# Optimization experiments

Hardware: AMD Instinct MI355X
Metric: run time of the kernel (lower is better)

Reference implementation:

```python
import jax, jax.numpy as jnp
import numpy as np

N = 4096
DIMS = {"word": 768, "pos": 64, "liwc": 93, "entity": 256, "text": 768}
HID, OUT = 256, 128
VIEWS = ["word", "pos", "liwc", "entity", "text"]


def setup_inputs() -> dict:
    key = jax.random.key(0)
    inp = {}
    for i, v in enumerate(VIEWS):
        ka, kx, k1, k2 = jax.random.split(jax.random.fold_in(key, i), 4)
        d = DIMS[v]
        # dense row-normalized adjacency surrogate
        a = jax.random.uniform(ka, (N, N), dtype=jnp.float32)
        inp[f"adj_{v}"] = a / jnp.sum(a, axis=1, keepdims=True)
        inp[f"x_{v}"] = jax.random.normal(kx, (N, d), dtype=jnp.float32)
        inp[f"W1_{v}"] = jax.random.normal(k1, (d, HID), dtype=jnp.float32) * (2.0 / (d + HID)) ** 0.5
        inp[f"b1_{v}"] = jnp.zeros((HID,), dtype=jnp.float32)
        inp[f"W2_{v}"] = jax.random.normal(k2, (HID, OUT), dtype=jnp.float32) * (2.0 / (HID + OUT)) ** 0.5
        inp[f"b2_{v}"] = jnp.zeros((OUT,), dtype=jnp.float32)
    return inp


def _gcn2(adj, x, W1, b1, W2, b2):
    # layer 1: adj @ (x @ W1) + b1, relu (dropout is identity in eval mode)
    h = jax.nn.relu(adj @ (x @ W1) + b1)
    # layer 2
    return adj @ (h @ W2) + b2


def reference(adj_word, adj_pos, adj_liwc, adj_entity, adj_text,
              x_word, x_pos, x_liwc, x_entity, x_text,
              W1_word, b1_word, W2_word, b2_word,
              W1_pos, b1_pos, W2_pos, b2_pos,
              W1_liwc, b1_liwc, W2_liwc, b2_liwc,
              W1_entity, b1_entity, W2_entity, b2_entity,
              W1_text, b1_text, W2_text, b2_text):
    return (
        _gcn2(adj_word, x_word, W1_word, b1_word, W2_word, b2_word),
        _gcn2(adj_pos, x_pos, W1_pos, b1_pos, W2_pos, b2_pos),
        _gcn2(adj_liwc, x_liwc, W1_liwc, b1_liwc, W2_liwc, b2_liwc),
        _gcn2(adj_entity, x_entity, W1_entity, b1_entity, W2_entity, b2_entity),
        _gcn2(adj_text, x_text, W1_text, b1_text, W2_text, b2_text),
    )
```

## Files before the change

### kernel.cpp

```cpp
#include <hip/hip_runtime.h>
#include <stdint.h>

typedef unsigned short u16;
typedef __attribute__((ext_vector_type(8))) __bf16 bf16x8;
typedef __attribute__((ext_vector_type(4))) float f32x4;
typedef __attribute__((ext_vector_type(4))) u16 u16x4;
typedef __attribute__((ext_vector_type(8))) u16 u16x8;

#define BM 128
#define BN 128
#define BK 32
#define MTOT 4096

__device__ __forceinline__ u16 f2bf(float f) {
  union { float f; uint32_t u; } x; x.f = f;
  uint32_t r = x.u + 0x7FFFu + ((x.u >> 16) & 1u);
  return (u16)(r >> 16);
}

__device__ __forceinline__ void gload16(const void* g, void* lds) {
  __builtin_amdgcn_global_load_lds(
      (const __attribute__((address_space(1))) void*)g,
      (__attribute__((address_space(3))) void*)lds, 16, 0, 0);
}

struct ViewParams {
  const void* A;
  const u16* BT;
  void* C;
  const float* bias;
  int K, lda, N;
};
struct Params5 { ViewParams v[5]; };

template <int FLAGS, bool AF32, bool CF32>
__global__ __launch_bounds__(256) void gemm_kernel(Params5 p, int tilesPerView, int ntiles) {
  constexpr int ABYTES = AF32 ? (BM * BK * 4) : (BM * BK * 2);
  __shared__ __align__(16) char smem[ABYTES + BN * BK * 2];
  u16* Bs = (u16*)(smem + ABYTES);

  const int bid = blockIdx.x;
  const int view = bid / tilesPerView;
  const int t = bid - view * tilesPerView;
  const int nt = t % ntiles;
  const int mt = t / ntiles;
  ViewParams vp = p.v[view];
  const int K = vp.K, lda = vp.lda, N = vp.N;
  const int m0 = mt * BM, n0 = nt * BN;

  const int tid = threadIdx.x;
  const int wave = tid >> 6;
  const int lane = tid & 63;

  const int srow = lane >> 2;
  const int slot4 = lane & 3;
  const int rB0 = wave * 32 + srow;
  const int rB1 = rB0 + 16;
  const int cB0 = slot4 ^ ((rB0 >> 1) & 3);
  const int cB1 = slot4 ^ ((rB1 >> 1) & 3);
  const u16* gB0 = vp.BT + (size_t)(n0 + rB0) * K + cB0 * 8;
  const u16* gB1 = vp.BT + (size_t)(n0 + rB1) * K + cB1 * 8;
  u16* lB0 = Bs + (wave * 32) * 32;
  u16* lB1 = Bs + (wave * 32 + 16) * 32;

  const float* gAf[4];
  float* lAf[4];
  const u16 *gAb0 = nullptr, *gAb1 = nullptr;
  u16 *lAb0 = nullptr, *lAb1 = nullptr;
  if constexpr (AF32) {
    const float* Af = (const float*)vp.A;
    const int arow = lane >> 3;
    const int slot8 = lane & 7;
#pragma unroll
    for (int i = 0; i < 4; i++) {
      int r = wave * 32 + i * 8 + arow;
      int c = slot8 ^ (r & 7);
      gAf[i] = Af + (size_t)(m0 + r) * lda + c * 4;
      lAf[i] = (float*)smem + (wave * 32 + i * 8) * 32;
    }
  } else {
    const u16* Ab = (const u16*)vp.A;
    const int rA0 = wave * 32 + srow;
    const int rA1 = rA0 + 16;
    const int cA0 = slot4 ^ ((rA0 >> 1) & 3);
    const int cA1 = slot4 ^ ((rA1 >> 1) & 3);
    gAb0 = Ab + (size_t)(m0 + rA0) * lda + cA0 * 8;
    gAb1 = Ab + (size_t)(m0 + rA1) * lda + cA1 * 8;
    lAb0 = (u16*)smem + (wave * 32) * 32;
    lAb1 = (u16*)smem + (wave * 32 + 16) * 32;
  }

  const int lm = lane & 15;
  const int q = lane >> 4;
  const int wm = (wave >> 1) * 64;
  const int wn = (wave & 1) * 64;
  int aoff0[4], aoff1[4], boff[4];
#pragma unroll
  for (int i = 0; i < 4; i++) {
    int ml = wm + i * 16 + lm;
    if constexpr (AF32) {
      aoff0[i] = ml * 32 + ((2 * q) ^ (ml & 7)) * 4;
      aoff1[i] = ml * 32 + ((2 * q + 1) ^ (ml & 7)) * 4;
    } else {
      aoff0[i] = ml * 32 + (q ^ ((ml >> 1) & 3)) * 8;
    }
    int nl = wn + i * 16 + lm;
    boff[i] = nl * 32 + (q ^ ((nl >> 1) & 3)) * 8;
  }

  f32x4 acc[4][4];
#pragma unroll
  for (int i = 0; i < 4; i++)
#pragma unroll
    for (int j = 0; j < 4; j++) acc[i][j] = 0.0f;

  for (int k0 = 0; k0 < K; k0 += BK) {
    if constexpr (AF32) {
#pragma unroll
      for (int i = 0; i < 4; i++) { gload16(gAf[i], lAf[i]); gAf[i] += BK; }
    } else {
      gload16(gAb0, lAb0); gload16(gAb1, lAb1);
      gAb0 += BK; gAb1 += BK;
    }
    gload16(gB0, lB0); gload16(gB1, lB1);
    gB0 += BK; gB1 += BK;
    __syncthreads();

    bf16x8 af[4], bfr[4];
#pragma unroll
    for (int i = 0; i < 4; i++) {
      if constexpr (AF32) {
        f32x4 lo = *(const f32x4*)((const float*)smem + aoff0[i]);
        f32x4 hi = *(const f32x4*)((const float*)smem + aoff1[i]);
        bf16x8 a;
#pragma unroll
        for (int tt = 0; tt < 4; tt++) { a[tt] = (__bf16)lo[tt]; a[tt + 4] = (__bf16)hi[tt]; }
        af[i] = a;
      } else {
        af[i] = *(const bf16x8*)((const u16*)smem + aoff0[i]);
      }
    }
#pragma unroll
    for (int j = 0; j < 4; j++) bfr[j] = *(const bf16x8*)(Bs + boff[j]);
#pragma unroll
    for (int i = 0; i < 4; i++)
#pragma unroll
      for (int j = 0; j < 4; j++)
        acc[i][j] = __builtin_amdgcn_mfma_f32_16x16x32_bf16(af[i], bfr[j], acc[i][j], 0, 0, 0);
    __syncthreads();
  }

#pragma unroll
  for (int j = 0; j < 4; j++) {
    const int n = n0 + wn + j * 16 + lm;
    float bv = 0.0f;
    if (FLAGS & 2) bv = vp.bias[n];
#pragma unroll
    for (int i = 0; i < 4; i++) {
      const int mb = m0 + wm + i * 16 + q * 4;
      float v0 = acc[i][j][0], v1 = acc[i][j][1], v2 = acc[i][j][2], v3 = acc[i][j][3];
      if (FLAGS & 2) { v0 += bv; v1 += bv; v2 += bv; v3 += bv; }
      if (FLAGS & 4) {
        v0 = fmaxf(v0, 0.0f); v1 = fmaxf(v1, 0.0f);
        v2 = fmaxf(v2, 0.0f); v3 = fmaxf(v3, 0.0f);
      }
      if constexpr ((FLAGS & 1) != 0) {
        u16x4 pk;
        pk[0] = f2bf(v0); pk[1] = f2bf(v1); pk[2] = f2bf(v2); pk[3] = f2bf(v3);
        *(u16x4*)((u16*)vp.C + (size_t)n * MTOT + mb) = pk;
      } else if constexpr (CF32) {
        float* cp = (float*)vp.C + (size_t)mb * N + n;
        cp[0] = v0; cp[N] = v1; cp[2 * N] = v2; cp[3 * N] = v3;
      } else {
        u16* cp = (u16*)vp.C + (size_t)mb * N + n;
        cp[0] = f2bf(v0); cp[N] = f2bf(v1); cp[2 * N] = f2bf(v2); cp[3 * N] = f2bf(v3);
      }
    }
  }
}

__global__ __launch_bounds__(256) void cvt_kernel(const float* __restrict__ in,
                                                  u16* __restrict__ out, long n8) {
  long i = (long)blockIdx.x * 256 + threadIdx.x;
  if (i >= n8) return;
  const f32x4* p = (const f32x4*)in + i * 2;
  f32x4 a = p[0], b = p[1];
  u16x8 o;
#pragma unroll
  for (int t = 0; t < 4; t++) { o[t] = f2bf(a[t]); o[t + 4] = f2bf(b[t]); }
  ((u16x8*)out)[i] = o;
}

struct PrepParams {
  const float* W1[5]; u16* W1T[5];
  const float* W2[5]; u16* W2T[5];
  const float* xl; float* xlp;
  int d[5]; int Kp[5];
};

__global__ void prep_kernel(PrepParams p, int total) {
  int idx = blockIdx.x * 256 + threadIdx.x;
  if (idx >= total) return;
  int off = 0;
#pragma unroll
  for (int v = 0; v < 5; v++) {
    int sz = 256 * p.Kp[v];
    if (idx < off + sz) {
      int r = idx - off;
      int n = r / p.Kp[v];
      int k = r - n * p.Kp[v];
      p.W1T[v][r] = (k < p.d[v]) ? f2bf(p.W1[v][(size_t)k * 256 + n]) : (u16)0;
      return;
    }
    off += sz;
  }
#pragma unroll
  for (int v = 0; v < 5; v++) {
    if (idx < off + 128 * 256) {
      int r = idx - off;
      int n = r >> 8, k = r & 255;
      p.W2T[v][r] = f2bf(p.W2[v][(size_t)k * 128 + n]);
      return;
    }
    off += 128 * 256;
  }
  {
    int r = idx - off;
    int m = r / 96, k = r - m * 96;
    p.xlp[r] = (k < 93) ? p.xl[(size_t)m * 93 + k] : 0.0f;
  }
}

extern "C" void kernel_launch(void* const* d_in, const int* in_sizes, int n_in,
                              void* d_out, int out_size, void* d_ws, size_t ws_size,
                              hipStream_t stream) {
  (void)in_sizes; (void)n_in; (void)out_size;
  static const int dims[5] = {768, 64, 93, 256, 768};
  static const int Kp[5]   = {768, 64, 96, 256, 768};

  const float *adjf[5], *xf[5], *W1f[5], *b1f[5], *W2f[5], *b2f[5];
  for (int v = 0; v < 5; v++) {
    adjf[v] = (const float*)d_in[6 * v + 0];
    xf[v]   = (const float*)d_in[6 * v + 1];
    W1f[v]  = (const float*)d_in[6 * v + 2];
    b1f[v]  = (const float*)d_in[6 * v + 3];
    W2f[v]  = (const float*)d_in[6 * v + 4];
    b2f[v]  = (const float*)d_in[6 * v + 5];
  }

  char* ws = (char*)d_ws;
  size_t off = 0;
  auto carve = [&](size_t bytes) { char* pp = ws + off; off += (bytes + 15) & ~(size_t)15; return pp; };
  u16* W1T[5]; for (int v = 0; v < 5; v++) W1T[v] = (u16*)carve((size_t)256 * Kp[v] * 2);
  u16* W2T[5]; for (int v = 0; v < 5; v++) W2T[v] = (u16*)carve((size_t)128 * 256 * 2);
  float* xlp = (float*)carve((size_t)4096 * 96 * 4);
  u16* Y1T[5]; for (int v = 0; v < 5; v++) Y1T[v] = (u16*)carve((size_t)256 * 4096 * 2);
  u16* HT[5];  for (int v = 0; v < 5; v++) HT[v]  = (u16*)carve((size_t)256 * 4096 * 2);
  u16* G[5];   for (int v = 0; v < 5; v++) G[v]   = (u16*)carve((size_t)4096 * 256 * 2);
  u16* adjb[5]; for (int v = 0; v < 5; v++) adjb[v] = (u16*)carve((size_t)4096 * 4096 * 2);
  const bool big = ws_size >= off;

  PrepParams pp;
  int prepTot = 0;
  for (int v = 0; v < 5; v++) {
    pp.W1[v] = W1f[v]; pp.W1T[v] = W1T[v];
    pp.W2[v] = W2f[v]; pp.W2T[v] = W2T[v];
    pp.d[v] = dims[v]; pp.Kp[v] = Kp[v];
    prepTot += 256 * Kp[v];
  }
  pp.xl = xf[2]; pp.xlp = xlp;
  prepTot += 5 * 128 * 256 + 4096 * 96;
  prep_kernel<<<(prepTot + 255) / 256, 256, 0, stream>>>(pp, prepTot);

  if (big) {
    const long n8 = (long)4096 * 4096 / 8;
    for (int v = 0; v < 5; v++)
      cvt_kernel<<<(int)(n8 / 256), 256, 0, stream>>>(adjf[v], adjb[v], n8);
  }

  Params5 pa;
  for (int v = 0; v < 5; v++)
    pa.v[v] = ViewParams{ (v == 2 ? (const void*)xlp : (const void*)xf[v]), W1T[v], Y1T[v],
                          nullptr, Kp[v], Kp[v], 256 };
  gemm_kernel<1, true, false><<<320, 256, 0, stream>>>(pa, 64, 2);

  Params5 pb;
  for (int v = 0; v < 5; v++)
    pb.v[v] = ViewParams{ big ? (const void*)adjb[v] : (const void*)adjf[v], Y1T[v], HT[v],
                          b1f[v], 4096, 4096, 256 };
  if (big) gemm_kernel<7, false, false><<<320, 256, 0, stream>>>(pb, 64, 2);
  else     gemm_kernel<7, true,  false><<<320, 256, 0, stream>>>(pb, 64, 2);

  Params5 pc;
  for (int v = 0; v < 5; v++)
    pc.v[v] = ViewParams{ big ? (const void*)adjb[v] : (const void*)adjf[v], HT[v], G[v],
                          nullptr, 4096, 4096, 256 };
  if (big) gemm_kernel<0, false, false><<<320, 256, 0, stream>>>(pc, 64, 2);
  else     gemm_kernel<0, true,  false><<<320, 256, 0, stream>>>(pc, 64, 2);

  Params5 pd;
  float* outp = (float*)d_out;
  for (int v = 0; v < 5; v++)
    pd.v[v] = ViewParams{ G[v], W2T[v], outp + (size_t)v * 4096 * 128, b2f[v], 256, 256, 128 };
  gemm_kernel<2, false, true><<<160, 256, 0, stream>>>(pd, 32, 1);
}
```

Baseline: 647.8 us.

## Split-K the adjacency GEMMs across two chunks and reduce partials in a combine kernel

The two 4096-deep adjacency GEMMs now split K into two halves, launching 640 blocks instead of 320 so more of the GPU's compute units are busy. Each half writes bf16 partial tiles, and a new combine kernel sums them and applies bias and ReLU. The five per-view fp32-to-bf16 adjacency conversions are merged into one launch. In exchange there is extra partial-buffer traffic, bf16 rounding of the partial sums, and two more launches. The fallback path without enough workspace is also changed to always read the bf16 adjacency copy.

After: 612.9 us. 1.06x faster.

```diff
diff --git a/kernel.cpp b/kernel.cpp
--- a/kernel.cpp
+++ b/kernel.cpp
@@ -17,6 +17,10 @@
   uint32_t r = x.u + 0x7FFFu + ((x.u >> 16) & 1u);
   return (u16)(r >> 16);
 }
+__device__ __forceinline__ float bf2f(u16 h) {
+  union { uint32_t u; float f; } x; x.u = ((uint32_t)h) << 16;
+  return x.f;
+}
 
 __device__ __forceinline__ void gload16(const void* g, void* lds) {
   __builtin_amdgcn_global_load_lds(
@@ -29,12 +33,15 @@
   const u16* BT;
   void* C;
   const float* bias;
-  int K, lda, N;
+  int ldab, lda, N;
+  int kspan;
+  size_t partStride;
 };
 struct Params5 { ViewParams v[5]; };
 
 template <int FLAGS, bool AF32, bool CF32>
-__global__ __launch_bounds__(256) void gemm_kernel(Params5 p, int tilesPerView, int ntiles) {
+__global__ __launch_bounds__(256) void gemm_kernel(Params5 p, int tilesPerView,
+                                                   int ntiles, int kchunks) {
   constexpr int ABYTES = AF32 ? (BM * BK * 4) : (BM * BK * 2);
   __shared__ __align__(16) char smem[ABYTES + BN * BK * 2];
   u16* Bs = (u16*)(smem + ABYTES);
@@ -42,11 +49,14 @@
   const int bid = blockIdx.x;
   const int view = bid / tilesPerView;
   const int t = bid - view * tilesPerView;
-  const int nt = t % ntiles;
-  const int mt = t / ntiles;
+  const int kc = t % kchunks;
+  const int t2 = t / kchunks;
+  const int nt = t2 % ntiles;
+  const int mt = t2 / ntiles;
   ViewParams vp = p.v[view];
-  const int K = vp.K, lda = vp.lda, N = vp.N;
+  const int ldab = vp.ldab, lda = vp.lda, N = vp.N;
   const int m0 = mt * BM, n0 = nt * BN;
+  const int kbase = kc * vp.kspan;
 
   const int tid = threadIdx.x;
   const int wave = tid >> 6;
@@ -58,8 +68,8 @@
   const int rB1 = rB0 + 16;
   const int cB0 = slot4 ^ ((rB0 >> 1) & 3);
   const int cB1 = slot4 ^ ((rB1 >> 1) & 3);
-  const u16* gB0 = vp.BT + (size_t)(n0 + rB0) * K + cB0 * 8;
-  const u16* gB1 = vp.BT + (size_t)(n0 + rB1) * K + cB1 * 8;
+  const u16* gB0 = vp.BT + (size_t)(n0 + rB0) * ldab + kbase + cB0 * 8;
+  const u16* gB1 = vp.BT + (size_t)(n0 + rB1) * ldab + kbase + cB1 * 8;
   u16* lB0 = Bs + (wave * 32) * 32;
   u16* lB1 = Bs + (wave * 32 + 16) * 32;
 
@@ -75,7 +85,7 @@
     for (int i = 0; i < 4; i++) {
       int r = wave * 32 + i * 8 + arow;
       int c = slot8 ^ (r & 7);
-      gAf[i] = Af + (size_t)(m0 + r) * lda + c * 4;
+      gAf[i] = Af + (size_t)(m0 + r) * lda + kbase + c * 4;
       lAf[i] = (float*)smem + (wave * 32 + i * 8) * 32;
     }
   } else {
@@ -84,8 +94,8 @@
     const int rA1 = rA0 + 16;
     const int cA0 = slot4 ^ ((rA0 >> 1) & 3);
     const int cA1 = slot4 ^ ((rA1 >> 1) & 3);
-    gAb0 = Ab + (size_t)(m0 + rA0) * lda + cA0 * 8;
-    gAb1 = Ab + (size_t)(m0 + rA1) * lda + cA1 * 8;
+    gAb0 = Ab + (size_t)(m0 + rA0) * lda + kbase + cA0 * 8;
+    gAb1 = Ab + (size_t)(m0 + rA1) * lda + kbase + cA1 * 8;
     lAb0 = (u16*)smem + (wave * 32) * 32;
     lAb1 = (u16*)smem + (wave * 32 + 16) * 32;
   }
@@ -114,7 +124,7 @@
 #pragma unroll
     for (int j = 0; j < 4; j++) acc[i][j] = 0.0f;
 
-  for (int k0 = 0; k0 < K; k0 += BK) {
+  for (int ks = 0; ks < vp.kspan; ks += BK) {
     if constexpr (AF32) {
 #pragma unroll
       for (int i = 0; i < 4; i++) { gload16(gAf[i], lAf[i]); gAf[i] += BK; }
@@ -167,28 +177,52 @@
       if constexpr ((FLAGS & 1) != 0) {
         u16x4 pk;
         pk[0] = f2bf(v0); pk[1] = f2bf(v1); pk[2] = f2bf(v2); pk[3] = f2bf(v3);
-        *(u16x4*)((u16*)vp.C + (size_t)n * MTOT + mb) = pk;
+        *(u16x4*)((u16*)vp.C + (size_t)kc * vp.partStride + (size_t)n * MTOT + mb) = pk;
       } else if constexpr (CF32) {
         float* cp = (float*)vp.C + (size_t)mb * N + n;
         cp[0] = v0; cp[N] = v1; cp[2 * N] = v2; cp[3 * N] = v3;
       } else {
-        u16* cp = (u16*)vp.C + (size_t)mb * N + n;
+        u16* cp = (u16*)vp.C + (size_t)kc * vp.partStride + (size_t)mb * N + n;
         cp[0] = f2bf(v0); cp[N] = f2bf(v1); cp[2 * N] = f2bf(v2); cp[3 * N] = f2bf(v3);
       }
     }
   }
 }
 
-__global__ __launch_bounds__(256) void cvt_kernel(const float* __restrict__ in,
-                                                  u16* __restrict__ out, long n8) {
+struct CvtParams { const float* src[5]; u16* dst; };
+__global__ __launch_bounds__(256) void cvt_kernel(CvtParams cp) {
   long i = (long)blockIdx.x * 256 + threadIdx.x;
-  if (i >= n8) return;
-  const f32x4* p = (const f32x4*)in + i * 2;
+  int v = (int)(i >> 21);
+  long r = i & ((1L << 21) - 1);
+  const f32x4* p = (const f32x4*)cp.src[v] + r * 2;
   f32x4 a = p[0], b = p[1];
   u16x8 o;
 #pragma unroll
   for (int t = 0; t < 4; t++) { o[t] = f2bf(a[t]); o[t + 4] = f2bf(b[t]); }
-  ((u16x8*)out)[i] = o;
+  ((u16x8*)cp.dst)[i] = o;
+}
+
+struct CombParams { const u16* parts; u16* out; const float* b[5]; int kchunks; };
+template <bool RELU>
+__global__ __launch_bounds__(256) void comb_kernel(CombParams cp) {
+  int idx = blockIdx.x * 256 + threadIdx.x;
+  int v = idx >> 17;
+  int e = (idx & 131071) << 3;
+  float acc[8] = {0, 0, 0, 0, 0, 0, 0, 0};
+  for (int kc = 0; kc < cp.kchunks; kc++) {
+    u16x8 t = *(const u16x8*)(cp.parts + (((size_t)(kc * 5 + v)) << 20) + e);
+#pragma unroll
+    for (int j = 0; j < 8; j++) acc[j] += bf2f(t[j]);
+  }
+  if (RELU) {
+    float bv = cp.b[v][e >> 12];
+#pragma unroll
+    for (int j = 0; j < 8; j++) acc[j] = fmaxf(acc[j] + bv, 0.0f);
+  }
+  u16x8 o;
+#pragma unroll
+  for (int j = 0; j < 8; j++) o[j] = f2bf(acc[j]);
+  *(u16x8*)(cp.out + (((size_t)v) << 20) + e) = o;
 }
 
 struct PrepParams {
@@ -248,17 +282,19 @@
     b2f[v]  = (const float*)d_in[6 * v + 5];
   }
 
+  const size_t VIEW = (size_t)256 * 4096;
   char* ws = (char*)d_ws;
   size_t off = 0;
   auto carve = [&](size_t bytes) { char* pp = ws + off; off += (bytes + 15) & ~(size_t)15; return pp; };
   u16* W1T[5]; for (int v = 0; v < 5; v++) W1T[v] = (u16*)carve((size_t)256 * Kp[v] * 2);
   u16* W2T[5]; for (int v = 0; v < 5; v++) W2T[v] = (u16*)carve((size_t)128 * 256 * 2);
   float* xlp = (float*)carve((size_t)4096 * 96 * 4);
-  u16* Y1T[5]; for (int v = 0; v < 5; v++) Y1T[v] = (u16*)carve((size_t)256 * 4096 * 2);
-  u16* HT[5];  for (int v = 0; v < 5; v++) HT[v]  = (u16*)carve((size_t)256 * 4096 * 2);
-  u16* G[5];   for (int v = 0; v < 5; v++) G[v]   = (u16*)carve((size_t)4096 * 256 * 2);
-  u16* adjb[5]; for (int v = 0; v < 5; v++) adjb[v] = (u16*)carve((size_t)4096 * 4096 * 2);
-  const bool big = ws_size >= off;
+  u16* Y1T = (u16*)carve(5 * VIEW * 2);
+  u16* PARTS = (u16*)carve(2 * 5 * VIEW * 2);
+  u16* HT = (u16*)carve(5 * VIEW * 2);
+  u16* adjb = (u16*)carve((size_t)5 * 4096 * 4096 * 2);
+  const bool ksplit = ws_size >= off;
+  u16* G = Y1T;
 
   PrepParams pp;
   int prepTot = 0;
@@ -272,35 +308,52 @@
   prepTot += 5 * 128 * 256 + 4096 * 96;
   prep_kernel<<<(prepTot + 255) / 256, 256, 0, stream>>>(pp, prepTot);
 
-  if (big) {
-    const long n8 = (long)4096 * 4096 / 8;
-    for (int v = 0; v < 5; v++)
-      cvt_kernel<<<(int)(n8 / 256), 256, 0, stream>>>(adjf[v], adjb[v], n8);
-  }
-
   Params5 pa;
   for (int v = 0; v < 5; v++)
-    pa.v[v] = ViewParams{ (v == 2 ? (const void*)xlp : (const void*)xf[v]), W1T[v], Y1T[v],
-                          nullptr, Kp[v], Kp[v], 256 };
-  gemm_kernel<1, true, false><<<320, 256, 0, stream>>>(pa, 64, 2);
-
-  Params5 pb;
-  for (int v = 0; v < 5; v++)
-    pb.v[v] = ViewParams{ big ? (const void*)adjb[v] : (const void*)adjf[v], Y1T[v], HT[v],
-                          b1f[v], 4096, 4096, 256 };
-  if (big) gemm_kernel<7, false, false><<<320, 256, 0, stream>>>(pb, 64, 2);
-  else     gemm_kernel<7, true,  false><<<320, 256, 0, stream>>>(pb, 64, 2);
-
-  Params5 pc;
-  for (int v = 0; v < 5; v++)
-    pc.v[v] = ViewParams{ big ? (const void*)adjb[v] : (const void*)adjf[v], HT[v], G[v],
-                          nullptr, 4096, 4096, 256 };
-  if (big) gemm_kernel<0, false, false><<<320, 256, 0, stream>>>(pc, 64, 2);
-  else     gemm_kernel<0, true,  false><<<320, 256, 0, stream>>>(pc, 64, 2);
+    pa.v[v] = ViewParams{ (v == 2 ? (const void*)xlp : (const void*)xf[v]), W1T[v], Y1T + v * VIEW,
+                          nullptr, Kp[v], Kp[v], 256, Kp[v], 0 };
+  gemm_kernel<1, true, false><<<320, 256, 0, stream>>>(pa, 64, 2, 1);
+
+  CvtParams cv;
+  for (int v = 0; v < 5; v++) cv.src[v] = adjf[v];
+  cv.dst = adjb;
+  cvt_kernel<<<40960, 256, 0, stream>>>(cv);
+
+  if (ksplit) {
+    Params5 pb;
+    for (int v = 0; v < 5; v++)
+      pb.v[v] = ViewParams{ adjb + (size_t)v * 4096 * 4096, Y1T + v * VIEW, PARTS + v * VIEW,
+                            nullptr, 4096, 4096, 256, 2048, 5 * VIEW };
+    gemm_kernel<1, false, false><<<640, 256, 0, stream>>>(pb, 128, 2, 2);
+
+    CombParams c1{ PARTS, HT, { b1f[0], b1f[1], b1f[2], b1f[3], b1f[4] }, 2 };
+    comb_kernel<true><<<2560, 256, 0, stream>>>(c1);
+
+    Params5 pc;
+    for (int v = 0; v < 5; v++)
+      pc.v[v] = ViewParams{ adjb + (size_t)v * 4096 * 4096, HT + v * VIEW, PARTS + v * VIEW,
+                            nullptr, 4096, 4096, 256, 2048, 5 * VIEW };
+    gemm_kernel<0, false, false><<<640, 256, 0, stream>>>(pc, 128, 2, 2);
+
+    CombParams c2{ PARTS, G, { nullptr, nullptr, nullptr, nullptr, nullptr }, 2 };
+    comb_kernel<false><<<2560, 256, 0, stream>>>(c2);
+  } else {
+    Params5 pb;
+    for (int v = 0; v < 5; v++)
+      pb.v[v] = ViewParams{ adjb + (size_t)v * 4096 * 4096, Y1T + v * VIEW, HT + v * VIEW,
+                            b1f[v], 4096, 4096, 256, 4096, 0 };
+    gemm_kernel<7, false, false><<<320, 256, 0, stream>>>(pb, 64, 2, 1);
+    Params5 pc;
+    for (int v = 0; v < 5; v++)
+      pc.v[v] = ViewParams{ adjb + (size_t)v * 4096 * 4096, HT + v * VIEW, G + v * VIEW,
+                            nullptr, 4096, 4096, 256, 4096, 0 };
+    gemm_kernel<0, false, false><<<320, 256, 0, stream>>>(pc, 64, 2, 1);
+  }
 
   Params5 pd;
   float* outp = (float*)d_out;
   for (int v = 0; v < 5; v++)
-    pd.v[v] = ViewParams{ G[v], W2T[v], outp + (size_t)v * 4096 * 128, b2f[v], 256, 256, 128 };
-  gemm_kernel<2, false, true><<<160, 256, 0, stream>>>(pd, 32, 1);
-}
+    pd.v[v] = ViewParams{ G + v * VIEW, W2T[v], outp + (size_t)v * 4096 * 128, b2f[v],
+                          256, 256, 128, 256, 0 };
+  gemm_kernel<2, false, true><<<160, 256, 0, stream>>>(pd, 32, 1, 1);
+}
```
